# Kernel optimization log

Hardware: AMD Instinct MI355X
Metric: run time of the kernel (lower is better)

The kernel has to match this reference:

```python
import jax, jax.numpy as jnp
import numpy as np

N_NODES = 50000
N_EDGES = 800000
IN_DIM = 128
HID = 256
OUT = 256


def setup_inputs() -> dict:
    key = jax.random.key(0)
    ks = jax.random.split(key, 16)
    s = 0.05
    return {
        "x": jax.random.normal(ks[0], (N_NODES, IN_DIM), jnp.float32),
        "edge_index": jax.random.randint(ks[1], (2, N_EDGES), 0, N_NODES),
        "W_gcn": jax.random.normal(ks[2], (IN_DIM, HID), jnp.float32) * s,
        "b_gcn": jnp.zeros((HID,), jnp.float32),
        "W_gat": jax.random.normal(ks[3], (IN_DIM, HID), jnp.float32) * s,
        "att_src": jax.random.normal(ks[4], (HID,), jnp.float32) * s,
        "att_dst": jax.random.normal(ks[5], (HID,), jnp.float32) * s,
        "b_gat": jnp.zeros((HID,), jnp.float32),
        "W_sage_l": jax.random.normal(ks[6], (IN_DIM, HID), jnp.float32) * s,
        "b_sage_l": jnp.zeros((HID,), jnp.float32),
        "W_sage_r": jax.random.normal(ks[7], (IN_DIM, HID), jnp.float32) * s,
        "W_fus": jax.random.normal(ks[8], (3 * HID, OUT), jnp.float32) * s,
        "b_fus": jnp.zeros((OUT,), jnp.float32),
    }


def reference(x, edge_index, W_gcn, b_gcn, W_gat, att_src, att_dst, b_gat,
              W_sage_l, b_sage_l, W_sage_r, W_fus, b_fus):
    N = x.shape[0]
    row, col = edge_index[0], edge_index[1]  # source -> target
    loop = jnp.arange(N)
    row_sl = jnp.concatenate([row, loop])  # with self-loops (GCN & GAT)
    col_sl = jnp.concatenate([col, loop])

    # ---- GCNConv: symmetric normalization, transform-then-propagate ----
    xg = x @ W_gcn  # [N, H]
    w = jnp.ones(row_sl.shape[0], x.dtype)
    deg = jax.ops.segment_sum(w, col_sl, num_segments=N)  # >= 1 due to self-loops
    dis = jax.lax.rsqrt(deg)
    norm = dis[row_sl] * dis[col_sl]  # [E+N]
    h_gcn = jax.ops.segment_sum(norm[:, None] * xg[row_sl], col_sl, num_segments=N) + b_gcn

    # ---- GATConv (1 head): attention softmax over incoming edges ----
    xa = x @ W_gat  # [N, H]
    a_src = xa @ att_src  # [N]
    a_dst = xa @ att_dst  # [N]
    e = jax.nn.leaky_relu(a_src[row_sl] + a_dst[col_sl], 0.2)  # [E+N]
    m = jax.ops.segment_max(e, col_sl, num_segments=N)  # per-target max (stable softmax)
    p = jnp.exp(e - m[col_sl])
    z = jax.ops.segment_sum(p, col_sl, num_segments=N)
    alpha = p / (z[col_sl] + 1e-16)
    h_gat = jax.ops.segment_sum(alpha[:, None] * xa[row_sl], col_sl, num_segments=N) + b_gat

    # ---- SAGEConv: mean neighbor aggregation (no self-loops) + root ----
    msum = jax.ops.segment_sum(x[row], col, num_segments=N)
    cnt = jax.ops.segment_sum(jnp.ones(row.shape[0], x.dtype), col, num_segments=N)
    mean = msum / jnp.maximum(cnt, 1.0)[:, None]
    h_sage = mean @ W_sage_l + b_sage_l + x @ W_sage_r

    h = jnp.concatenate([jax.nn.relu(h_gcn), jax.nn.relu(h_gat), jax.nn.relu(h_sage)], axis=1)
    return h @ W_fus + b_fus
```

## Files before the change

kernel.cpp:

```cpp
#include <hip/hip_runtime.h>
#include <hip/hip_bf16.h>

typedef __hip_bfloat16 bf16;
typedef short bf16x8 __attribute__((ext_vector_type(8)));
typedef float f32x4  __attribute__((ext_vector_type(4)));

static constexpr int D_IN  = 128;
static constexpr int D_H   = 256;
static constexpr int D_CAT = 768;

__device__ __forceinline__ float lrelu(float v){ return v > 0.f ? v : 0.2f*v; }
__device__ __forceinline__ float b2f(bf16 v){ return __bfloat162float(v); }
__device__ __forceinline__ bf16  f2b(float v){ return __float2bfloat16(v); }
__device__ __forceinline__ unsigned packb(float lo, float hi){
  bf16 a = f2b(lo), b = f2b(hi);
  unsigned short ua, ub;
  __builtin_memcpy(&ua, &a, 2); __builtin_memcpy(&ub, &b, 2);
  return (unsigned)ua | ((unsigned)ub << 16);
}
__device__ __forceinline__ short bbits(float v){
  bf16 h = f2b(v); short s; __builtin_memcpy(&s, &h, 2); return s;
}

__device__ __forceinline__ void gload_lds16(const void* g, void* l){
  __builtin_amdgcn_global_load_lds(
      (const __attribute__((address_space(1))) unsigned*)g,
      (__attribute__((address_space(3))) unsigned*)l, 16, 0, 0);
}

__global__ __launch_bounds__(256) void k_count(const int* __restrict__ col,
                                               int* __restrict__ cnt, int E){
  int e = blockIdx.x*256 + threadIdx.x;
  if (e < E) atomicAdd(&cnt[col[e]], 1);
}

__global__ __launch_bounds__(256) void k_scanA(const int* __restrict__ cnt,
                                               int* __restrict__ indptr,
                                               int* __restrict__ bsum, int N){
  __shared__ int s[256];
  int t = threadIdx.x, i = blockIdx.x*256 + t;
  int v = (i < N) ? cnt[i] : 0;
  s[t] = v; __syncthreads();
  #pragma unroll
  for (int d = 1; d < 256; d <<= 1){
    int tmp = (t >= d) ? s[t-d] : 0;
    __syncthreads();
    s[t] += tmp;
    __syncthreads();
  }
  if (i < N) indptr[i] = s[t] - v;
  if (t == 255) bsum[blockIdx.x] = s[255];
}

__global__ __launch_bounds__(256) void k_scanB(const int* __restrict__ bsum,
                                               int* __restrict__ boff,
                                               int* __restrict__ indptr,
                                               int nb, int N, int E){
  __shared__ int s[256];
  int t = threadIdx.x;
  int v = (t < nb) ? bsum[t] : 0;
  s[t] = v; __syncthreads();
  #pragma unroll
  for (int d = 1; d < 256; d <<= 1){
    int tmp = (t >= d) ? s[t-d] : 0;
    __syncthreads();
    s[t] += tmp;
    __syncthreads();
  }
  boff[t] = s[t] - v;
  if (t == 0) indptr[N] = E;
}

__global__ __launch_bounds__(256) void k_scanC(int* __restrict__ indptr,
                                               const int* __restrict__ boff, int N){
  int i = blockIdx.x*256 + threadIdx.x;
  if (i < N) indptr[i] += boff[blockIdx.x];
}

__global__ __launch_bounds__(256) void k_dis(const int* __restrict__ cnt,
                                             float* __restrict__ dis, int N){
  int i = blockIdx.x*256 + threadIdx.x;
  if (i < N) dis[i] = rsqrtf((float)cnt[i] + 1.0f);
}

__global__ __launch_bounds__(256) void k_fill(const int* __restrict__ row,
                                              const int* __restrict__ col,
                                              const int* __restrict__ indptr,
                                              int* __restrict__ cursor,
                                              int* __restrict__ esrc, int E){
  int e = blockIdx.x*256 + threadIdx.x;
  if (e < E){
    int c = col[e];
    int p = indptr[c] + atomicAdd(&cursor[c], 1);
    esrc[p] = row[e];
  }
}

__global__ __launch_bounds__(256) void k_cast(const float* __restrict__ x,
                                              bf16* __restrict__ xb, int n4){
  int i = blockIdx.x*256 + threadIdx.x;
  if (i < n4){
    float4 v = reinterpret_cast<const float4*>(x)[i];
    bf16* o = xb + (size_t)i*4;
    o[0]=f2b(v.x); o[1]=f2b(v.y); o[2]=f2b(v.z); o[3]=f2b(v.w);
  }
}

__global__ __launch_bounds__(128) void k_wvec(const float* __restrict__ W_gat,
                                              const float* __restrict__ att_src,
                                              const float* __restrict__ att_dst,
                                              float* __restrict__ wsrc,
                                              float* __restrict__ wdst){
  int k = threadIdx.x;
  float s1 = 0.f, s2 = 0.f;
  for (int j = 0; j < D_H; ++j){
    float w = W_gat[(size_t)k*D_H + j];
    s1 = fmaf(w, att_src[j], s1);
    s2 = fmaf(w, att_dst[j], s2);
  }
  wsrc[k] = s1; wdst[k] = s2;
}

__global__ __launch_bounds__(256) void k_packW1(const float* __restrict__ Wg,
                                                const float* __restrict__ Wa,
                                                const float* __restrict__ Wl,
                                                const float* __restrict__ Wr,
                                                bf16* __restrict__ W1t){
  int n = blockIdx.x, k = threadIdx.x;
  float v = 0.f;
  if (n < 256)      { if (k < 128)  v = Wg[(size_t)k*D_H + n]; }
  else if (n < 512) { if (k >= 128) v = Wa[(size_t)(k-128)*D_H + (n-256)]; }
  else              { v = (k < 128) ? Wl[(size_t)k*D_H + (n-512)]
                                    : Wr[(size_t)(k-128)*D_H + (n-512)]; }
  W1t[(size_t)n*256 + k] = f2b(v);
}

__global__ __launch_bounds__(256) void k_packF(const float* __restrict__ W,
                                               bf16* __restrict__ Bt){
  int n = blockIdx.x;
  for (int k = threadIdx.x; k < D_CAT; k += 256)
    Bt[(size_t)n*D_CAT + k] = f2b(W[(size_t)k*D_H + n]);
}

__global__ __launch_bounds__(256) void k_bias3(const float* __restrict__ bg,
                                               const float* __restrict__ ba,
                                               const float* __restrict__ bs,
                                               float* __restrict__ out){
  int i = blockIdx.x*256 + threadIdx.x;
  if (i < 256)      out[i] = bg[i];
  else if (i < 512) out[i] = ba[i-256];
  else if (i < 768) out[i] = bs[i-512];
}

__global__ __launch_bounds__(256) void k_asrc(const bf16* __restrict__ xb,
                                              const float* __restrict__ wsrc,
                                              const float* __restrict__ wdst,
                                              float* __restrict__ a_src,
                                              float* __restrict__ a_dst, int N){
  int w = threadIdx.x >> 6, l = threadIdx.x & 63;
  int c = blockIdx.x*4 + w;
  if (c >= N) return;
  unsigned u = *(const unsigned*)(xb + (size_t)c*D_IN + 2*l);
  float x0 = __uint_as_float(u << 16);
  float x1 = __uint_as_float(u & 0xffff0000u);
  float s1 = x0*wsrc[2*l] + x1*wsrc[2*l+1];
  float s2 = x0*wdst[2*l] + x1*wdst[2*l+1];
  #pragma unroll
  for (int o = 32; o > 0; o >>= 1){
    s1 += __shfl_down(s1, o);
    s2 += __shfl_down(s2, o);
  }
  if (l == 0){ a_src[c] = s1; a_dst[c] = s2; }
}

__global__ __launch_bounds__(256) void k_aggx(
    const int* __restrict__ indptr, const int* __restrict__ esrc,
    const bf16* __restrict__ xb,
    const float* __restrict__ a_src, const float* __restrict__ a_dst,
    const float* __restrict__ dis,
    bf16* __restrict__ AGG, int N)
{
  int c = blockIdx.x;
  if (c >= N) return;
  int t = threadIdx.x;
  int beg = indptr[c], end = indptr[c+1];
  int deg = end - beg;
  float adst = a_dst[c], dc = dis[c];
  float eself = lrelu(a_src[c] + adst);

  __shared__ int   s_src[256];
  __shared__ float s_pe[256];
  __shared__ float s_ds[256];
  __shared__ float pg[4][128], pa[4][128], ps[4][128];
  __shared__ float red[4];

  float lm = eself;
  for (int e = beg + t; e < end; e += 256)
    lm = fmaxf(lm, lrelu(a_src[esrc[e]] + adst));
  #pragma unroll
  for (int o = 32; o > 0; o >>= 1) lm = fmaxf(lm, __shfl_down(lm, o));
  if ((t & 63) == 0) red[t >> 6] = lm;
  __syncthreads();
  float m = fmaxf(fmaxf(red[0], red[1]), fmaxf(red[2], red[3]));

  float p0 = __expf(eself - m);
  float z_loc = (t == 0) ? p0 : 0.f;

  int d2 = t & 63;
  int g  = t >> 6;
  float g0=0.f,g1=0.f,a0=0.f,a1=0.f,sg0=0.f,sg1=0.f;

  for (int ch0 = beg; ch0 < end; ch0 += 256){
    int n = min(256, end - ch0);
    __syncthreads();
    if (t < n){
      int s = esrc[ch0 + t];
      float pe = __expf(lrelu(a_src[s] + adst) - m);
      s_src[t] = s; s_pe[t] = pe; s_ds[t] = dis[s];
      z_loc += pe;
    }
    __syncthreads();
    int i = g;
    for (; i + 12 < n; i += 16){
      int sA = s_src[i],    sB = s_src[i+4],
          sC = s_src[i+8],  sD = s_src[i+12];
      unsigned uA = *(const unsigned*)(xb + (size_t)sA*D_IN + 2*d2);
      unsigned uB = *(const unsigned*)(xb + (size_t)sB*D_IN + 2*d2);
      unsigned uC = *(const unsigned*)(xb + (size_t)sC*D_IN + 2*d2);
      unsigned uD = *(const unsigned*)(xb + (size_t)sD*D_IN + 2*d2);
      float peA = s_pe[i],   dsA = s_ds[i];
      float peB = s_pe[i+4], dsB = s_ds[i+4];
      float peC = s_pe[i+8], dsC = s_ds[i+8];
      float peD = s_pe[i+12],dsD = s_ds[i+12];
      float xA0 = __uint_as_float(uA << 16), xA1 = __uint_as_float(uA & 0xffff0000u);
      float xB0 = __uint_as_float(uB << 16), xB1 = __uint_as_float(uB & 0xffff0000u);
      float xC0 = __uint_as_float(uC << 16), xC1 = __uint_as_float(uC & 0xffff0000u);
      float xD0 = __uint_as_float(uD << 16), xD1 = __uint_as_float(uD & 0xffff0000u);
      g0 = fmaf(dsA,xA0,g0); g1 = fmaf(dsA,xA1,g1);
      a0 = fmaf(peA,xA0,a0); a1 = fmaf(peA,xA1,a1);
      sg0 += xA0; sg1 += xA1;
      g0 = fmaf(dsB,xB0,g0); g1 = fmaf(dsB,xB1,g1);
      a0 = fmaf(peB,xB0,a0); a1 = fmaf(peB,xB1,a1);
      sg0 += xB0; sg1 += xB1;
      g0 = fmaf(dsC,xC0,g0); g1 = fmaf(dsC,xC1,g1);
      a0 = fmaf(peC,xC0,a0); a1 = fmaf(peC,xC1,a1);
      sg0 += xC0; sg1 += xC1;
      g0 = fmaf(dsD,xD0,g0); g1 = fmaf(dsD,xD1,g1);
      a0 = fmaf(peD,xD0,a0); a1 = fmaf(peD,xD1,a1);
      sg0 += xD0; sg1 += xD1;
    }
    for (; i < n; i += 4){
      int s = s_src[i];
      float pe = s_pe[i], ds = s_ds[i];
      unsigned u = *(const unsigned*)(xb + (size_t)s*D_IN + 2*d2);
      float x0 = __uint_as_float(u << 16);
      float x1 = __uint_as_float(u & 0xffff0000u);
      g0 = fmaf(ds, x0, g0); g1 = fmaf(ds, x1, g1);
      a0 = fmaf(pe, x0, a0); a1 = fmaf(pe, x1, a1);
      sg0 += x0; sg1 += x1;
    }
  }

  #pragma unroll
  for (int o = 32; o > 0; o >>= 1) z_loc += __shfl_down(z_loc, o);
  __syncthreads();
  if ((t & 63) == 0) red[t >> 6] = z_loc;
  __syncthreads();
  float z = red[0] + red[1] + red[2] + red[3];

  pg[g][2*d2] = g0; pg[g][2*d2+1] = g1;
  pa[g][2*d2] = a0; pa[g][2*d2+1] = a1;
  ps[g][2*d2] = sg0; ps[g][2*d2+1] = sg1;
  __syncthreads();

  if (t < 64){
    int d0 = 2*t, d1 = 2*t + 1;
    float G0 = pg[0][d0]+pg[1][d0]+pg[2][d0]+pg[3][d0];
    float G1 = pg[0][d1]+pg[1][d1]+pg[2][d1]+pg[3][d1];
    float A0 = pa[0][d0]+pa[1][d0]+pa[2][d0]+pa[3][d0];
    float A1 = pa[0][d1]+pa[1][d1]+pa[2][d1]+pa[3][d1];
    float S0 = ps[0][d0]+ps[1][d0]+ps[2][d0]+ps[3][d0];
    float S1 = ps[0][d1]+ps[1][d1]+ps[2][d1]+ps[3][d1];
    unsigned xu = *(const unsigned*)(xb + (size_t)c*D_IN + d0);
    float xc0 = __uint_as_float(xu << 16);
    float xc1 = __uint_as_float(xu & 0xffff0000u);
    float invz = 1.f / (z + 1e-16f);
    float invc = 1.f / fmaxf((float)deg, 1.f);
    unsigned* rowp = (unsigned*)(AGG + (size_t)c*512);
    rowp[t]        = packb(dc*(G0 + dc*xc0), dc*(G1 + dc*xc1));
    rowp[64 + t]   = packb((A0 + p0*xc0)*invz, (A1 + p0*xc1)*invz);
    rowp[128 + t]  = packb(S0*invc, S1*invc);
    rowp[192 + t]  = xu;
  }
}

__global__ __launch_bounds__(512, 4) void k_mlp(
    const bf16* __restrict__ AGG,
    const bf16* __restrict__ W1t,
    const bf16* __restrict__ W2t,
    const float* __restrict__ bias1,
    const float* __restrict__ bias2,
    float* __restrict__ out, int M)
{
  __shared__ short A_res[4*64*64];
  __shared__ short Hc[2*64*64];
  __shared__ short SW[256*64];
  int tid  = threadIdx.x;
  int bm   = blockIdx.x*64;
  int wave = tid >> 6, lane = tid & 63;
  int l15  = lane & 15, l4 = lane >> 4;
  int wr   = (wave >> 2)*32;
  int wcol = wave & 3;

  f32x4 oacc[2][4] = {};

  #pragma unroll
  for (int i = 0; i < 4; ++i){
    int slot = i*512 + tid;
    int rr = (slot >> 3) & 63, gp = slot & 7;
    int gk = gp ^ (rr & 7);
    int p  = slot >> 9;
    int row = bm + rr; if (row >= M) row = M - 1;
    gload_lds16(AGG + (size_t)row*512 + p*64 + gk*8, A_res + (size_t)slot*8);
  }

  #pragma unroll
  for (int j = 0; j < 6; ++j){
    if (j == 4){
      #pragma unroll
      for (int i = 0; i < 4; ++i){
        int slot = i*512 + tid;
        int rr = (slot >> 3) & 63, gp = slot & 7;
        int gk = gp ^ (rr & 7);
        int p  = slot >> 9;
        int row = bm + rr; if (row >= M) row = M - 1;
        gload_lds16(AGG + (size_t)row*512 + 256 + p*64 + gk*8, A_res + (size_t)slot*8);
      }
    }
    const int p0 = (j < 2) ? 0 : ((j < 4) ? 2 : 0);
    const int np = (j < 4) ? 2 : 4;
    f32x4 hacc[2][2] = {};
    for (int pp = 0; pp < np; ++pp){
      int p = p0 + pp;
      __syncthreads();
      #pragma unroll
      for (int i = 0; i < 2; ++i){
        int slot = i*512 + tid;
        int r = slot >> 3, gp = slot & 7;
        int gk = gp ^ (r & 7);
        gload_lds16(W1t + (size_t)(j*128 + r)*256 + p*64 + gk*8, SW + (size_t)slot*8);
      }
      __syncthreads();
      #pragma unroll
      for (int kk = 0; kk < 2; ++kk){
        bf16x8 af[2], bfv[2];
        #pragma unroll
        for (int mi = 0; mi < 2; ++mi){
          int r = wr + mi*16 + l15;
          int gk = kk*4 + l4;
          af[mi] = *(const bf16x8*)(A_res + p*4096 + r*64 + ((gk ^ (r & 7))*8));
        }
        #pragma unroll
        for (int ni = 0; ni < 2; ++ni){
          int r = wcol*32 + ni*16 + l15;
          int gk = kk*4 + l4;
          bfv[ni] = *(const bf16x8*)(SW + r*64 + ((gk ^ (r & 7))*8));
        }
        #pragma unroll
        for (int mi = 0; mi < 2; ++mi)
          #pragma unroll
          for (int ni = 0; ni < 2; ++ni)
            hacc[mi][ni] = __builtin_amdgcn_mfma_f32_16x16x32_bf16(
                               af[mi], bfv[ni], hacc[mi][ni], 0, 0, 0);
      }
    }
    #pragma unroll
    for (int mi = 0; mi < 2; ++mi)
      #pragma unroll
      for (int ni = 0; ni < 2; ++ni){
        int cc = wcol*32 + ni*16 + l15;
        float bb = bias1[j*128 + cc];
        int q = cc >> 6, g8 = (cc >> 3) & 7, e = cc & 7;
        #pragma unroll
        for (int r = 0; r < 4; ++r){
          int rr = wr + mi*16 + l4*4 + r;
          float v = fmaxf(hacc[mi][ni][r] + bb, 0.f);
          Hc[q*4096 + rr*64 + ((g8 ^ (rr & 7))*8) + e] = bbits(v);
        }
      }
    #pragma unroll
    for (int q = 0; q < 2; ++q){
      __syncthreads();
      #pragma unroll
      for (int i = 0; i < 4; ++i){
        int slot = i*512 + tid;
        int r = slot >> 3, gp = slot & 7;
        int gk = gp ^ (r & 7);
        gload_lds16(W2t + (size_t)r*768 + j*128 + q*64 + gk*8, SW + (size_t)slot*8);
      }
      __syncthreads();
      #pragma unroll
      for (int kk = 0; kk < 2; ++kk){
        bf16x8 af[2], bfv[4];
        #pragma unroll
        for (int mi = 0; mi < 2; ++mi){
          int r = wr + mi*16 + l15;
          int gk = kk*4 + l4;
          af[mi] = *(const bf16x8*)(Hc + q*4096 + r*64 + ((gk ^ (r & 7))*8));
        }
        #pragma unroll
        for (int ni = 0; ni < 4; ++ni){
          int r = wcol*64 + ni*16 + l15;
          int gk = kk*4 + l4;
          bfv[ni] = *(const bf16x8*)(SW + r*64 + ((gk ^ (r & 7))*8));
        }
        #pragma unroll
        for (int mi = 0; mi < 2; ++mi)
          #pragma unroll
          for (int ni = 0; ni < 4; ++ni)
            oacc[mi][ni] = __builtin_amdgcn_mfma_f32_16x16x32_bf16(
                               af[mi], bfv[ni], oacc[mi][ni], 0, 0, 0);
      }
    }
  }

  #pragma unroll
  for (int mi = 0; mi < 2; ++mi)
    #pragma unroll
    for (int r = 0; r < 4; ++r){
      int row = bm + wr + mi*16 + l4*4 + r;
      if (row >= M) continue;
      #pragma unroll
      for (int ni = 0; ni < 4; ++ni){
        int col = wcol*64 + ni*16 + l15;
        out[(size_t)row*256 + col] = oacc[mi][ni][r] + bias2[col];
      }
    }
}

static inline char* carve(char*& p, size_t bytes){
  char* r = p;
  p += (bytes + 255) & ~(size_t)255;
  return r;
}

extern "C" void kernel_launch(void* const* d_in, const int* in_sizes, int n_in,
                              void* d_out, int out_size, void* d_ws, size_t ws_size,
                              hipStream_t stream) {
  const float* x        = (const float*)d_in[0];
  const int*   ei       = (const int*)  d_in[1];
  const float* W_gcn    = (const float*)d_in[2];
  const float* b_gcn    = (const float*)d_in[3];
  const float* W_gat    = (const float*)d_in[4];
  const float* att_src  = (const float*)d_in[5];
  const float* att_dst  = (const float*)d_in[6];
  const float* b_gat    = (const float*)d_in[7];
  const float* W_sage_l = (const float*)d_in[8];
  const float* b_sage_l = (const float*)d_in[9];
  const float* W_sage_r = (const float*)d_in[10];
  const float* W_fus    = (const float*)d_in[11];
  const float* b_fus    = (const float*)d_in[12];

  const int N = in_sizes[0] / D_IN;
  const int E = in_sizes[1] / 2;
  const int* erow = ei;
  const int* ecol = ei + E;

  char* p = (char*)d_ws;
  bf16*  AGG    = (bf16*) carve(p, (size_t)N*512*2);
  bf16*  xb     = (bf16*) carve(p, (size_t)N*D_IN*2);
  bf16*  W1t    = (bf16*) carve(p, (size_t)D_CAT*256*2);
  bf16*  W2t    = (bf16*) carve(p, (size_t)256*D_CAT*2);
  float* bias1  = (float*)carve(p, D_CAT*4);
  float* wsrc   = (float*)carve(p, D_IN*4);
  float* wdst   = (float*)carve(p, D_IN*4);
  float* a_src  = (float*)carve(p, (size_t)N*4);
  float* a_dst  = (float*)carve(p, (size_t)N*4);
  float* dis    = (float*)carve(p, (size_t)N*4);
  int*   cnt    = (int*)  carve(p, (size_t)N*4);
  int*   cursor = (int*)  carve(p, (size_t)N*4);
  int*   indptr = (int*)  carve(p, (size_t)(N+1)*4);
  int*   bsum   = (int*)  carve(p, 256*4);
  int*   boff   = (int*)  carve(p, 256*4);
  int*   esrc   = (int*)  carve(p, (size_t)E*4);
  (void)ws_size; (void)n_in; (void)out_size;

  hipMemsetAsync(cnt,    0, (size_t)N*4, stream);
  hipMemsetAsync(cursor, 0, (size_t)N*4, stream);

  const int nb = (N + 255) / 256;
  const int eb = (E + 255) / 256;

  k_cast  <<<(N*D_IN/4 + 255)/256, 256, 0, stream>>>(x, xb, N*D_IN/4);
  k_wvec  <<<1, 128, 0, stream>>>(W_gat, att_src, att_dst, wsrc, wdst);
  k_packW1<<<D_CAT, 256, 0, stream>>>(W_gcn, W_gat, W_sage_l, W_sage_r, W1t);
  k_packF <<<256, 256, 0, stream>>>(W_fus, W2t);
  k_bias3 <<<3, 256, 0, stream>>>(b_gcn, b_gat, b_sage_l, bias1);

  k_count<<<eb, 256, 0, stream>>>(ecol, cnt, E);
  k_scanA<<<nb, 256, 0, stream>>>(cnt, indptr, bsum, N);
  k_scanB<<<1, 256, 0, stream>>>(bsum, boff, indptr, nb, N, E);
  k_scanC<<<nb, 256, 0, stream>>>(indptr, boff, N);
  k_dis  <<<nb, 256, 0, stream>>>(cnt, dis, N);
  k_fill <<<eb, 256, 0, stream>>>(erow, ecol, indptr, cursor, esrc, E);

  k_asrc<<<(N + 3)/4, 256, 0, stream>>>(xb, wsrc, wdst, a_src, a_dst, N);

  k_aggx<<<N, 256, 0, stream>>>(indptr, esrc, xb, a_src, a_dst, dis, AGG, N);

  k_mlp<<<(N + 63)/64, 512, 0, stream>>>(AGG, W1t, W2t, bias1, b_fus,
                                         (float*)d_out, N);
}
```

Baseline: 375.0 us.

## Fuse prep kernels, compute GAT max via atomics in fill, widen gather unroll

Merges the weight packing, bias copy, attention-vector and edge-count kernels into one launch, and fuses the bf16 cast of x into the attention-logit kernel. The degree rsqrt moves into the scan, so the separate dis kernel goes away. The per-target softmax max is now built during CSR fill with an order-preserving float encoding and atomicMax on a_src, since leaky_relu is monotone; this removes a full pass over each node's edges in the aggregation kernel. The gather loop is also unrolled to 8 loads in flight. The cost is extra atomics in fill and higher register use in the gather loop.

```diff
diff --git a/kernel.cpp b/kernel.cpp
--- a/kernel.cpp
+++ b/kernel.cpp
@@ -10,7 +10,6 @@
 static constexpr int D_CAT = 768;
 
 __device__ __forceinline__ float lrelu(float v){ return v > 0.f ? v : 0.2f*v; }
-__device__ __forceinline__ float b2f(bf16 v){ return __bfloat162float(v); }
 __device__ __forceinline__ bf16  f2b(float v){ return __float2bfloat16(v); }
 __device__ __forceinline__ unsigned packb(float lo, float hi){
   bf16 a = f2b(lo), b = f2b(hi);
@@ -21,6 +20,14 @@
 __device__ __forceinline__ short bbits(float v){
   bf16 h = f2b(v); short s; __builtin_memcpy(&s, &h, 2); return s;
 }
+__device__ __forceinline__ unsigned fenc(float f){
+  unsigned u = __float_as_uint(f);
+  return (u & 0x80000000u) ? ~u : (u | 0x80000000u);
+}
+__device__ __forceinline__ float fdec(unsigned e){
+  unsigned u = (e & 0x80000000u) ? (e ^ 0x80000000u) : ~e;
+  return __uint_as_float(u);
+}
 
 __device__ __forceinline__ void gload_lds16(const void* g, void* l){
   __builtin_amdgcn_global_load_lds(
@@ -28,15 +35,76 @@
       (__attribute__((address_space(3))) unsigned*)l, 16, 0, 0);
 }
 
-__global__ __launch_bounds__(256) void k_count(const int* __restrict__ col,
-                                               int* __restrict__ cnt, int E){
-  int e = blockIdx.x*256 + threadIdx.x;
-  if (e < E) atomicAdd(&cnt[col[e]], 1);
+__global__ __launch_bounds__(256) void k_prep(
+    const float* __restrict__ Wg, const float* __restrict__ Wa,
+    const float* __restrict__ Wl, const float* __restrict__ Wr,
+    const float* __restrict__ Wf,
+    const float* __restrict__ att_src, const float* __restrict__ att_dst,
+    const float* __restrict__ bg, const float* __restrict__ ba,
+    const float* __restrict__ bs,
+    const int* __restrict__ ecol,
+    bf16* __restrict__ W1t, bf16* __restrict__ W2t,
+    float* __restrict__ bias1, float* __restrict__ wsrc,
+    float* __restrict__ wdst, int* __restrict__ cnt, int E)
+{
+  int b = blockIdx.x, t = threadIdx.x;
+  if (b < 768){
+    int n = b, k = t;
+    float v = 0.f;
+    if (n < 256)      { if (k < 128)  v = Wg[(size_t)k*D_H + n]; }
+    else if (n < 512) { if (k >= 128) v = Wa[(size_t)(k-128)*D_H + (n-256)]; }
+    else              { v = (k < 128) ? Wl[(size_t)k*D_H + (n-512)]
+                                      : Wr[(size_t)(k-128)*D_H + (n-512)]; }
+    W1t[(size_t)n*256 + k] = f2b(v);
+  } else if (b < 1024){
+    int n = b - 768;
+    for (int k = t; k < D_CAT; k += 256)
+      W2t[(size_t)n*D_CAT + k] = f2b(Wf[(size_t)k*D_H + n]);
+  } else if (b == 1024){
+    bias1[t] = bg[t]; bias1[256+t] = ba[t]; bias1[512+t] = bs[t];
+  } else if (b == 1025){
+    if (t < 128){
+      float s1 = 0.f, s2 = 0.f;
+      for (int j = 0; j < D_H; ++j){
+        float w = Wa[(size_t)t*D_H + j];
+        s1 = fmaf(w, att_src[j], s1);
+        s2 = fmaf(w, att_dst[j], s2);
+      }
+      wsrc[t] = s1; wdst[t] = s2;
+    }
+  } else {
+    int e = (b - 1026)*256 + t;
+    if (e < E) atomicAdd(&cnt[ecol[e]], 1);
+  }
+}
+
+__global__ __launch_bounds__(256) void k_asrc(const float* __restrict__ x,
+                                              const float* __restrict__ wsrc,
+                                              const float* __restrict__ wdst,
+                                              bf16* __restrict__ xb,
+                                              float* __restrict__ a_src,
+                                              float* __restrict__ a_dst,
+                                              unsigned* __restrict__ maxenc,
+                                              int N){
+  int w = threadIdx.x >> 6, l = threadIdx.x & 63;
+  int c = blockIdx.x*4 + w;
+  if (c >= N) return;
+  float2 xv = *(const float2*)(x + (size_t)c*D_IN + 2*l);
+  *(unsigned*)(xb + (size_t)c*D_IN + 2*l) = packb(xv.x, xv.y);
+  float s1 = xv.x*wsrc[2*l] + xv.y*wsrc[2*l+1];
+  float s2 = xv.x*wdst[2*l] + xv.y*wdst[2*l+1];
+  #pragma unroll
+  for (int o = 32; o > 0; o >>= 1){
+    s1 += __shfl_down(s1, o);
+    s2 += __shfl_down(s2, o);
+  }
+  if (l == 0){ a_src[c] = s1; a_dst[c] = s2; maxenc[c] = fenc(s1); }
 }
 
 __global__ __launch_bounds__(256) void k_scanA(const int* __restrict__ cnt,
                                                int* __restrict__ indptr,
-                                               int* __restrict__ bsum, int N){
+                                               int* __restrict__ bsum,
+                                               float* __restrict__ dis, int N){
   __shared__ int s[256];
   int t = threadIdx.x, i = blockIdx.x*256 + t;
   int v = (i < N) ? cnt[i] : 0;
@@ -48,7 +116,10 @@
     s[t] += tmp;
     __syncthreads();
   }
-  if (i < N) indptr[i] = s[t] - v;
+  if (i < N){
+    indptr[i] = s[t] - v;
+    dis[i] = rsqrtf((float)v + 1.0f);
+  }
   if (t == 255) bsum[blockIdx.x] = s[255];
 }
 
@@ -77,100 +148,21 @@
   if (i < N) indptr[i] += boff[blockIdx.x];
 }
 
-__global__ __launch_bounds__(256) void k_dis(const int* __restrict__ cnt,
-                                             float* __restrict__ dis, int N){
-  int i = blockIdx.x*256 + threadIdx.x;
-  if (i < N) dis[i] = rsqrtf((float)cnt[i] + 1.0f);
-}
-
 __global__ __launch_bounds__(256) void k_fill(const int* __restrict__ row,
                                               const int* __restrict__ col,
                                               const int* __restrict__ indptr,
                                               int* __restrict__ cursor,
-                                              int* __restrict__ esrc, int E){
+                                              int* __restrict__ esrc,
+                                              const float* __restrict__ a_src,
+                                              unsigned* __restrict__ maxenc,
+                                              int E){
   int e = blockIdx.x*256 + threadIdx.x;
   if (e < E){
-    int c = col[e];
+    int r = row[e], c = col[e];
     int p = indptr[c] + atomicAdd(&cursor[c], 1);
-    esrc[p] = row[e];
-  }
-}
-
-__global__ __launch_bounds__(256) void k_cast(const float* __restrict__ x,
-                                              bf16* __restrict__ xb, int n4){
-  int i = blockIdx.x*256 + threadIdx.x;
-  if (i < n4){
-    float4 v = reinterpret_cast<const float4*>(x)[i];
-    bf16* o = xb + (size_t)i*4;
-    o[0]=f2b(v.x); o[1]=f2b(v.y); o[2]=f2b(v.z); o[3]=f2b(v.w);
-  }
-}
-
-__global__ __launch_bounds__(128) void k_wvec(const float* __restrict__ W_gat,
-                                              const float* __restrict__ att_src,
-                                              const float* __restrict__ att_dst,
-                                              float* __restrict__ wsrc,
-                                              float* __restrict__ wdst){
-  int k = threadIdx.x;
-  float s1 = 0.f, s2 = 0.f;
-  for (int j = 0; j < D_H; ++j){
-    float w = W_gat[(size_t)k*D_H + j];
-    s1 = fmaf(w, att_src[j], s1);
-    s2 = fmaf(w, att_dst[j], s2);
-  }
-  wsrc[k] = s1; wdst[k] = s2;
-}
-
-__global__ __launch_bounds__(256) void k_packW1(const float* __restrict__ Wg,
-                                                const float* __restrict__ Wa,
-                                                const float* __restrict__ Wl,
-                                                const float* __restrict__ Wr,
-                                                bf16* __restrict__ W1t){
-  int n = blockIdx.x, k = threadIdx.x;
-  float v = 0.f;
-  if (n < 256)      { if (k < 128)  v = Wg[(size_t)k*D_H + n]; }
-  else if (n < 512) { if (k >= 128) v = Wa[(size_t)(k-128)*D_H + (n-256)]; }
-  else              { v = (k < 128) ? Wl[(size_t)k*D_H + (n-512)]
-                                    : Wr[(size_t)(k-128)*D_H + (n-512)]; }
-  W1t[(size_t)n*256 + k] = f2b(v);
-}
-
-__global__ __launch_bounds__(256) void k_packF(const float* __restrict__ W,
-                                               bf16* __restrict__ Bt){
-  int n = blockIdx.x;
-  for (int k = threadIdx.x; k < D_CAT; k += 256)
-    Bt[(size_t)n*D_CAT + k] = f2b(W[(size_t)k*D_H + n]);
-}
-
-__global__ __launch_bounds__(256) void k_bias3(const float* __restrict__ bg,
-                                               const float* __restrict__ ba,
-                                               const float* __restrict__ bs,
-                                               float* __restrict__ out){
-  int i = blockIdx.x*256 + threadIdx.x;
-  if (i < 256)      out[i] = bg[i];
-  else if (i < 512) out[i] = ba[i-256];
-  else if (i < 768) out[i] = bs[i-512];
-}
-
-__global__ __launch_bounds__(256) void k_asrc(const bf16* __restrict__ xb,
-                                              const float* __restrict__ wsrc,
-                                              const float* __restrict__ wdst,
-                                              float* __restrict__ a_src,
-                                              float* __restrict__ a_dst, int N){
-  int w = threadIdx.x >> 6, l = threadIdx.x & 63;
-  int c = blockIdx.x*4 + w;
-  if (c >= N) return;
-  unsigned u = *(const unsigned*)(xb + (size_t)c*D_IN + 2*l);
-  float x0 = __uint_as_float(u << 16);
-  float x1 = __uint_as_float(u & 0xffff0000u);
-  float s1 = x0*wsrc[2*l] + x1*wsrc[2*l+1];
-  float s2 = x0*wdst[2*l] + x1*wdst[2*l+1];
-  #pragma unroll
-  for (int o = 32; o > 0; o >>= 1){
-    s1 += __shfl_down(s1, o);
-    s2 += __shfl_down(s2, o);
-  }
-  if (l == 0){ a_src[c] = s1; a_dst[c] = s2; }
+    esrc[p] = r;
+    atomicMax(&maxenc[c], fenc(a_src[r]));
+  }
 }
 
 __global__ __launch_bounds__(256) void k_aggx(
@@ -178,6 +170,7 @@
     const bf16* __restrict__ xb,
     const float* __restrict__ a_src, const float* __restrict__ a_dst,
     const float* __restrict__ dis,
+    const unsigned* __restrict__ maxenc,
     bf16* __restrict__ AGG, int N)
 {
   int c = blockIdx.x;
@@ -187,6 +180,7 @@
   int deg = end - beg;
   float adst = a_dst[c], dc = dis[c];
   float eself = lrelu(a_src[c] + adst);
+  float m = lrelu(fdec(maxenc[c]) + adst);
 
   __shared__ int   s_src[256];
   __shared__ float s_pe[256];
@@ -194,15 +188,6 @@
   __shared__ float pg[4][128], pa[4][128], ps[4][128];
   __shared__ float red[4];
 
-  float lm = eself;
-  for (int e = beg + t; e < end; e += 256)
-    lm = fmaxf(lm, lrelu(a_src[esrc[e]] + adst));
-  #pragma unroll
-  for (int o = 32; o > 0; o >>= 1) lm = fmaxf(lm, __shfl_down(lm, o));
-  if ((t & 63) == 0) red[t >> 6] = lm;
-  __syncthreads();
-  float m = fmaxf(fmaxf(red[0], red[1]), fmaxf(red[2], red[3]));
-
   float p0 = __expf(eself - m);
   float z_loc = (t == 0) ? p0 : 0.f;
 
@@ -221,33 +206,23 @@
     }
     __syncthreads();
     int i = g;
-    for (; i + 12 < n; i += 16){
-      int sA = s_src[i],    sB = s_src[i+4],
-          sC = s_src[i+8],  sD = s_src[i+12];
-      unsigned uA = *(const unsigned*)(xb + (size_t)sA*D_IN + 2*d2);
-      unsigned uB = *(const unsigned*)(xb + (size_t)sB*D_IN + 2*d2);
-      unsigned uC = *(const unsigned*)(xb + (size_t)sC*D_IN + 2*d2);
-      unsigned uD = *(const unsigned*)(xb + (size_t)sD*D_IN + 2*d2);
-      float peA = s_pe[i],   dsA = s_ds[i];
-      float peB = s_pe[i+4], dsB = s_ds[i+4];
-      float peC = s_pe[i+8], dsC = s_ds[i+8];
-      float peD = s_pe[i+12],dsD = s_ds[i+12];
-      float xA0 = __uint_as_float(uA << 16), xA1 = __uint_as_float(uA & 0xffff0000u);
-      float xB0 = __uint_as_float(uB << 16), xB1 = __uint_as_float(uB & 0xffff0000u);
-      float xC0 = __uint_as_float(uC << 16), xC1 = __uint_as_float(uC & 0xffff0000u);
-      float xD0 = __uint_as_float(uD << 16), xD1 = __uint_as_float(uD & 0xffff0000u);
-      g0 = fmaf(dsA,xA0,g0); g1 = fmaf(dsA,xA1,g1);
-      a0 = fmaf(peA,xA0,a0); a1 = fmaf(peA,xA1,a1);
-      sg0 += xA0; sg1 += xA1;
-      g0 = fmaf(dsB,xB0,g0); g1 = fmaf(dsB,xB1,g1);
-      a0 = fmaf(peB,xB0,a0); a1 = fmaf(peB,xB1,a1);
-      sg0 += xB0; sg1 += xB1;
-      g0 = fmaf(dsC,xC0,g0); g1 = fmaf(dsC,xC1,g1);
-      a0 = fmaf(peC,xC0,a0); a1 = fmaf(peC,xC1,a1);
-      sg0 += xC0; sg1 += xC1;
-      g0 = fmaf(dsD,xD0,g0); g1 = fmaf(dsD,xD1,g1);
-      a0 = fmaf(peD,xD0,a0); a1 = fmaf(peD,xD1,a1);
-      sg0 += xD0; sg1 += xD1;
+    for (; i + 28 < n; i += 32){
+      unsigned u[8]; float pe[8], ds[8];
+      #pragma unroll
+      for (int q = 0; q < 8; ++q){
+        int s = s_src[i + 4*q];
+        u[q] = *(const unsigned*)(xb + (size_t)s*D_IN + 2*d2);
+      }
+      #pragma unroll
+      for (int q = 0; q < 8; ++q){ pe[q] = s_pe[i+4*q]; ds[q] = s_ds[i+4*q]; }
+      #pragma unroll
+      for (int q = 0; q < 8; ++q){
+        float x0 = __uint_as_float(u[q] << 16);
+        float x1 = __uint_as_float(u[q] & 0xffff0000u);
+        g0 = fmaf(ds[q], x0, g0); g1 = fmaf(ds[q], x1, g1);
+        a0 = fmaf(pe[q], x0, a0); a1 = fmaf(pe[q], x1, a1);
+        sg0 += x0; sg1 += x1;
+      }
     }
     for (; i < n; i += 4){
       int s = s_src[i];
@@ -263,7 +238,6 @@
 
   #pragma unroll
   for (int o = 32; o > 0; o >>= 1) z_loc += __shfl_down(z_loc, o);
-  __syncthreads();
   if ((t & 63) == 0) red[t >> 6] = z_loc;
   __syncthreads();
   float z = red[0] + red[1] + red[2] + red[3];
@@ -467,22 +441,23 @@
   const int* ecol = ei + E;
 
   char* p = (char*)d_ws;
-  bf16*  AGG    = (bf16*) carve(p, (size_t)N*512*2);
-  bf16*  xb     = (bf16*) carve(p, (size_t)N*D_IN*2);
-  bf16*  W1t    = (bf16*) carve(p, (size_t)D_CAT*256*2);
-  bf16*  W2t    = (bf16*) carve(p, (size_t)256*D_CAT*2);
-  float* bias1  = (float*)carve(p, D_CAT*4);
-  float* wsrc   = (float*)carve(p, D_IN*4);
-  float* wdst   = (float*)carve(p, D_IN*4);
-  float* a_src  = (float*)carve(p, (size_t)N*4);
-  float* a_dst  = (float*)carve(p, (size_t)N*4);
-  float* dis    = (float*)carve(p, (size_t)N*4);
-  int*   cnt    = (int*)  carve(p, (size_t)N*4);
-  int*   cursor = (int*)  carve(p, (size_t)N*4);
-  int*   indptr = (int*)  carve(p, (size_t)(N+1)*4);
-  int*   bsum   = (int*)  carve(p, 256*4);
-  int*   boff   = (int*)  carve(p, 256*4);
-  int*   esrc   = (int*)  carve(p, (size_t)E*4);
+  bf16*     AGG    = (bf16*)    carve(p, (size_t)N*512*2);
+  bf16*     xb     = (bf16*)    carve(p, (size_t)N*D_IN*2);
+  bf16*     W1t    = (bf16*)    carve(p, (size_t)D_CAT*256*2);
+  bf16*     W2t    = (bf16*)    carve(p, (size_t)256*D_CAT*2);
+  float*    bias1  = (float*)   carve(p, D_CAT*4);
+  float*    wsrc   = (float*)   carve(p, D_IN*4);
+  float*    wdst   = (float*)   carve(p, D_IN*4);
+  float*    a_src  = (float*)   carve(p, (size_t)N*4);
+  float*    a_dst  = (float*)   carve(p, (size_t)N*4);
+  float*    dis    = (float*)   carve(p, (size_t)N*4);
+  unsigned* maxenc = (unsigned*)carve(p, (size_t)N*4);
+  int*      cnt    = (int*)     carve(p, (size_t)N*4);
+  int*      cursor = (int*)     carve(p, (size_t)N*4);
+  int*      indptr = (int*)     carve(p, (size_t)(N+1)*4);
+  int*      bsum   = (int*)     carve(p, 256*4);
+  int*      boff   = (int*)     carve(p, 256*4);
+  int*      esrc   = (int*)     carve(p, (size_t)E*4);
   (void)ws_size; (void)n_in; (void)out_size;
 
   hipMemsetAsync(cnt,    0, (size_t)N*4, stream);
@@ -491,22 +466,21 @@
   const int nb = (N + 255) / 256;
   const int eb = (E + 255) / 256;
 
-  k_cast  <<<(N*D_IN/4 + 255)/256, 256, 0, stream>>>(x, xb, N*D_IN/4);
-  k_wvec  <<<1, 128, 0, stream>>>(W_gat, att_src, att_dst, wsrc, wdst);
-  k_packW1<<<D_CAT, 256, 0, stream>>>(W_gcn, W_gat, W_sage_l, W_sage_r, W1t);
-  k_packF <<<256, 256, 0, stream>>>(W_fus, W2t);
-  k_bias3 <<<3, 256, 0, stream>>>(b_gcn, b_gat, b_sage_l, bias1);
-
-  k_count<<<eb, 256, 0, stream>>>(ecol, cnt, E);
-  k_scanA<<<nb, 256, 0, stream>>>(cnt, indptr, bsum, N);
+  k_prep<<<1026 + eb, 256, 0, stream>>>(W_gcn, W_gat, W_sage_l, W_sage_r, W_fus,
+                                        att_src, att_dst, b_gcn, b_gat, b_sage_l,
+                                        ecol, W1t, W2t, bias1, wsrc, wdst, cnt, E);
+
+  k_asrc<<<(N + 3)/4, 256, 0, stream>>>(x, wsrc, wdst, xb, a_src, a_dst,
+                                        maxenc, N);
+
+  k_scanA<<<nb, 256, 0, stream>>>(cnt, indptr, bsum, dis, N);
   k_scanB<<<1, 256, 0, stream>>>(bsum, boff, indptr, nb, N, E);
   k_scanC<<<nb, 256, 0, stream>>>(indptr, boff, N);
-  k_dis  <<<nb, 256, 0, stream>>>(cnt, dis, N);
-  k_fill <<<eb, 256, 0, stream>>>(erow, ecol, indptr, cursor, esrc, E);
-
-  k_asrc<<<(N + 3)/4, 256, 0, stream>>>(xb, wsrc, wdst, a_src, a_dst, N);
-
-  k_aggx<<<N, 256, 0, stream>>>(indptr, esrc, xb, a_src, a_dst, dis, AGG, N);
+  k_fill <<<eb, 256, 0, stream>>>(erow, ecol, indptr, cursor, esrc,
+                                  a_src, maxenc, E);
+
+  k_aggx<<<N, 256, 0, stream>>>(indptr, esrc, xb, a_src, a_dst, dis,
+                                maxenc, AGG, N);
 
   k_mlp<<<(N + 63)/64, 512, 0, stream>>>(AGG, W1t, W2t, bias1, b_fus,
                                          (float*)d_out, N);
```

Result: slower. 392.8 us (+4.8%).
